# Kernel optimization log

Hardware: AMD Instinct MI355X
Metric: run time of the kernel (lower is better)

The kernel has to match this reference:

```python
import jax, jax.numpy as jnp
import numpy as np


def setup_inputs() -> dict:
    key = jax.random.key(0)
    ks = jax.random.split(key, 7)
    B, S, H, T = 128, 512, 768, 3
    return {
        "inputs": jax.random.normal(ks[0], (B, S, H), dtype=jnp.float32),
        "y": jax.random.randint(ks[1], (B, S), 0, T, dtype=jnp.int64),
        "W": jax.random.normal(ks[2], (T, H), dtype=jnp.float32) * 0.02,
        "b": jax.random.normal(ks[3], (T,), dtype=jnp.float32) * 0.02,
        "transitions": jax.random.normal(ks[4], (T, T), dtype=jnp.float32),
        "start_transitions": jax.random.normal(ks[5], (T,), dtype=jnp.float32),
        "stop_transitions": jax.random.normal(ks[6], (T,), dtype=jnp.float32),
    }


def _crf_loss(feats, tags, transitions, start_transitions, stop_transitions):
    # feats: (B, S, T) emissions; tags: (B, S) int labels
    B, S, T = feats.shape
    # ---- gold sequence score ----
    emit = jnp.take_along_axis(feats, tags[:, :, None], axis=2)[..., 0]  # (B, S)
    trans = transitions[tags[:, :-1], tags[:, 1:]]                        # (B, S-1)
    seq_score = (emit.sum(-1) + trans.sum(-1)
                 + start_transitions[tags[:, 0]]
                 + stop_transitions[tags[:, -1]])                          # (B,)
    # ---- log partition via forward algorithm (scan over time) ----
    a0 = feats[:, 0] + start_transitions[None, :]  # (B, T)

    def step(a, feat_t):
        # a: (B, T) alpha at t-1; feat_t: (B, T) emissions at t
        # scores[b, i, j] = a[b, i] + transitions[i, j] + feat_t[b, j]
        a_new = jax.nn.logsumexp(a[:, :, None] + transitions[None, :, :]
                                 + feat_t[:, None, :], axis=1)
        return a_new, None

    aT, _ = jax.lax.scan(step, a0, jnp.swapaxes(feats[:, 1:], 0, 1))
    log_z = jax.nn.logsumexp(aT + stop_transitions[None, :], axis=1)  # (B,)
    return -(seq_score - log_z).mean()


def reference(inputs, y, W, b, transitions, start_transitions, stop_transitions):
    # Linear projection: (B, S, H) @ (H, T) + (T,)
    prediction = jnp.einsum("bsh,th->bst", inputs, W) + b
    crf_loss = _crf_loss(prediction, y, transitions, start_transitions,
                         stop_transitions)
    return (prediction, crf_loss)
```

## Files before the change

kernel.cpp:

```cpp
#include <hip/hip_runtime.h>

constexpr int NB = 128;
constexpr int NS = 512;
constexpr int NH = 768;
constexpr int NT = 3;
constexpr int ROWS = NB * NS;
constexpr int NCH = 64;
constexpr int CHL = 8;
constexpr float NEG = -1e30f;

__device__ __forceinline__ float lse3(float x0, float x1, float x2) {
    float m = fmaxf(x0, fmaxf(x1, x2));
    return m + __logf(__expf(x0 - m) + __expf(x1 - m) + __expf(x2 - m));
}

__device__ __forceinline__ float dot4(float4 a, float4 b) {
    return a.x * b.x + a.y * b.y + a.z * b.z + a.w * b.w;
}

__device__ __forceinline__ float sel3(int t, float a, float b, float c) {
    return (t == 0) ? a : ((t == 1) ? b : c);
}

__global__ __launch_bounds__(256) void pred_kernel(
    const float* __restrict__ x, const float* __restrict__ W,
    const float* __restrict__ bias, float* __restrict__ out)
{
    const int lane = threadIdx.x & 63;
    const int gw   = blockIdx.x * 4 + (threadIdx.x >> 6);
    const int nw   = gridDim.x * 4;
    const int stride = nw * 2;

    const float4* W4 = (const float4*)W;
    float4 w[3][3];
#pragma unroll
    for (int t = 0; t < 3; ++t)
#pragma unroll
        for (int c = 0; c < 3; ++c)
            w[t][c] = W4[t * 192 + c * 64 + lane];
    const float b0 = bias[0], b1 = bias[1], b2 = bias[2];

    const float4* X4 = (const float4*)x;
    int row = gw * 2;
    if (row >= ROWS) return;

    float4 vA[3], vB[3];
    {
        const int ba = row * 192 + lane;
#pragma unroll
        for (int c = 0; c < 3; ++c) { vA[c] = X4[ba + c * 64]; vB[c] = X4[ba + 192 + c * 64]; }
    }

    while (true) {
        const int nrow = row + stride;
        const bool more = nrow < ROWS;
        float4 tA[3], tB[3];
        if (more) {
            const int nb = nrow * 192 + lane;
#pragma unroll
            for (int c = 0; c < 3; ++c) { tA[c] = X4[nb + c * 64]; tB[c] = X4[nb + 192 + c * 64]; }
        }
        float a0 = dot4(vA[0], w[0][0]) + dot4(vA[1], w[0][1]) + dot4(vA[2], w[0][2]);
        float a1 = dot4(vA[0], w[1][0]) + dot4(vA[1], w[1][1]) + dot4(vA[2], w[1][2]);
        float a2 = dot4(vA[0], w[2][0]) + dot4(vA[1], w[2][1]) + dot4(vA[2], w[2][2]);
        float c0 = dot4(vB[0], w[0][0]) + dot4(vB[1], w[0][1]) + dot4(vB[2], w[0][2]);
        float c1 = dot4(vB[0], w[1][0]) + dot4(vB[1], w[1][1]) + dot4(vB[2], w[1][2]);
        float c2 = dot4(vB[0], w[2][0]) + dot4(vB[1], w[2][1]) + dot4(vB[2], w[2][2]);

        float r0 = a0 + __shfl_xor(a0, 32, 64);
        float s0 = c0 + __shfl_xor(c0, 32, 64);
        float w0 = (lane & 32) ? s0 : r0;
        float r1 = a1 + __shfl_xor(a1, 32, 64);
        float s1 = c1 + __shfl_xor(c1, 32, 64);
        float w1 = (lane & 32) ? s1 : r1;
        float r2 = a2 + __shfl_xor(a2, 32, 64);
        float s2 = c2 + __shfl_xor(c2, 32, 64);
        float w2 = (lane & 32) ? s2 : r2;
        float p0 = w0 + __shfl_xor(w0, 16, 64);
        float p1 = w1 + __shfl_xor(w1, 16, 64);
        float z  = (lane & 16) ? p1 : p0;
#pragma unroll
        for (int off = 8; off >= 1; off >>= 1)
            z += __shfl_xor(z, off, 64);
#pragma unroll
        for (int off = 16; off >= 1; off >>= 1)
            w2 += __shfl_xor(w2, off, 64);

        if ((lane & 15) == 0) {
            const int t = (lane >> 4) & 1;
            const int r = lane >> 5;
            out[(size_t)row * 3 + r * 3 + t] = z + ((t == 0) ? b0 : b1);
        }
        if ((lane & 31) == 0) {
            const int r = lane >> 5;
            out[(size_t)row * 3 + r * 3 + 2] = w2 + b2;
        }
        if (!more) break;
#pragma unroll
        for (int c = 0; c < 3; ++c) { vA[c] = tA[c]; vB[c] = tB[c]; }
        row = nrow;
    }
}

__global__ __launch_bounds__(256) void crf_scan_kernel(
    const float* __restrict__ feats, const int* __restrict__ y,
    const float* __restrict__ trans, float* __restrict__ ws_m,
    float* __restrict__ ws_p)
{
    __shared__ float sTr[9];
    if (threadIdx.x < 9) sTr[threadIdx.x] = trans[threadIdx.x];
    __syncthreads();

    const int gtid = blockIdx.x * 256 + threadIdx.x;
    const int e  = gtid % 3;
    const int bc = gtid / 3;
    const int b  = bc >> 6;
    const int c  = bc & 63;

    const float T00 = sTr[0], T01 = sTr[1], T02 = sTr[2];
    const float T10 = sTr[3], T11 = sTr[4], T12 = sTr[5];
    const float T20 = sTr[6], T21 = sTr[7], T22 = sTr[8];

    const float* fb = feats + (size_t)b * NS * NT;
    const int*   yb = y + b * NS;

    float ff[24];
    {
        float4* fv = (float4*)ff;
        const float4* src = (const float4*)(fb + c * CHL * NT);
#pragma unroll
        for (int i = 0; i < 6; ++i) fv[i] = src[i];
    }
    int yy[8];
    {
        int4* yv = (int4*)yy;
        const int4* ys = (const int4*)(yb + c * CHL);
        yv[0] = ys[0]; yv[1] = ys[1];
    }

    float a0 = (e == 0) ? 0.f : NEG;
    float a1 = (e == 1) ? 0.f : NEG;
    float a2 = (e == 2) ? 0.f : NEG;

    float sc = 0.f;
    int prev;
    if (c == 0) {
        prev = yy[0];
        sc = sel3(prev, ff[0], ff[1], ff[2]);
    } else {
        prev = yb[c * CHL - 1];
    }
    const int sl0 = (c == 0) ? 1 : 0;

#pragma unroll
    for (int sl = 0; sl < CHL; ++sl) {
        if (sl < sl0) continue;
        const float f0 = ff[sl * 3], f1 = ff[sl * 3 + 1], f2 = ff[sl * 3 + 2];
        const int tg = yy[sl];
        sc += sel3(tg, f0, f1, f2) + sTr[prev * 3 + tg];
        prev = tg;
        const float n0 = f0 + lse3(a0 + T00, a1 + T10, a2 + T20);
        const float n1 = f1 + lse3(a0 + T01, a1 + T11, a2 + T21);
        const float n2 = f2 + lse3(a0 + T02, a1 + T12, a2 + T22);
        a0 = n0; a1 = n1; a2 = n2;
    }

    float4* dst = (float4*)(ws_m + (size_t)(b * NCH + c) * 12) + e;
    *dst = make_float4(a0, a1, a2, 0.f);
    if (e == 0) ws_p[b * NCH + c] = sc;
}

__global__ __launch_bounds__(128) void crf_combine_kernel(
    const float* __restrict__ feats, const int* __restrict__ y,
    const float* __restrict__ ws_m, const float* __restrict__ ws_p,
    const float* __restrict__ startt, const float* __restrict__ stopt,
    float* __restrict__ loss_out)
{
    __shared__ float partial[2];
    const int b = threadIdx.x;

    const float st0 = startt[0], st1 = startt[1], st2 = startt[2];
    const float sp0 = stopt[0],  sp1 = stopt[1],  sp2 = stopt[2];

    const float* fb = feats + (size_t)b * NS * NT;
    float a0 = fb[0] + st0, a1 = fb[1] + st1, a2 = fb[2] + st2;

    const float4* M = (const float4*)(ws_m + (size_t)b * NCH * 12);
    const float*  P = ws_p + b * NCH;

    float4 m0 = M[0], m1 = M[1], m2 = M[2];
    float  pp = P[0];
    float  sc = 0.f;

#pragma unroll 4
    for (int c = 0; c < NCH; ++c) {
        float4 u0 = m0, u1 = m1, u2 = m2; float up = pp;
        if (c < NCH - 1) {
            u0 = M[(c + 1) * 3]; u1 = M[(c + 1) * 3 + 1]; u2 = M[(c + 1) * 3 + 2];
            up = P[c + 1];
        }
        sc += pp;
        const float n0 = lse3(a0 + m0.x, a1 + m1.x, a2 + m2.x);
        const float n1 = lse3(a0 + m0.y, a1 + m1.y, a2 + m2.y);
        const float n2 = lse3(a0 + m0.z, a1 + m1.z, a2 + m2.z);
        a0 = n0; a1 = n1; a2 = n2;
        m0 = u0; m1 = u1; m2 = u2; pp = up;
    }

    const float logz = lse3(a0 + sp0, a1 + sp1, a2 + sp2);
    const int y0 = y[b * NS], yl = y[b * NS + NS - 1];
    const float seq = sc + ((y0 == 0) ? st0 : ((y0 == 1) ? st1 : st2))
                         + ((yl == 0) ? sp0 : ((yl == 1) ? sp1 : sp2));
    float val = seq - logz;

#pragma unroll
    for (int off = 32; off >= 1; off >>= 1)
        val += __shfl_xor(val, off, 64);
    if ((threadIdx.x & 63) == 0) partial[threadIdx.x >> 6] = val;
    __syncthreads();
    if (threadIdx.x == 0)
        loss_out[0] = -(partial[0] + partial[1]) / (float)NB;
}

extern "C" void kernel_launch(void* const* d_in, const int* in_sizes, int n_in,
                              void* d_out, int out_size, void* d_ws, size_t ws_size,
                              hipStream_t stream)
{
    const float* x      = (const float*)d_in[0];
    const int*   y      = (const int*)d_in[1];
    const float* W      = (const float*)d_in[2];
    const float* bias   = (const float*)d_in[3];
    const float* trans  = (const float*)d_in[4];
    const float* startt = (const float*)d_in[5];
    const float* stopt  = (const float*)d_in[6];

    float* out      = (float*)d_out;
    float* loss_out = out + (size_t)NB * NS * NT;

    float* ws_m = (float*)d_ws;
    float* ws_p = ws_m + (size_t)NB * NCH * 12;

    pred_kernel<<<1024, 256, 0, stream>>>(x, W, bias, out);
    crf_scan_kernel<<<(NB * NCH * 3) / 256, 256, 0, stream>>>(out, y, trans, ws_m, ws_p);
    crf_combine_kernel<<<1, 128, 0, stream>>>(out, y, ws_m, ws_p, startt, stopt, loss_out);
}
```

Before: 320.9 us.

## Fuse CRF chunk scan and combine into one per-batch kernel with atomic loss

Merges the chunked CRF forward scan and the single-block combine into one kernel with one block per batch row. Chunk transfer matrices now stay in shared memory instead of a global workspace. Each block reduces its row serially and adds its share of the loss with an atomicAdd, and pred_kernel zeroes the loss first. This removes a kernel launch and the workspace round trip, but the loss sum order now varies between runs and each block does a serial 64-step combine on one thread.

After: 306.2 us. 1.05x faster.

```diff
diff --git a/kernel.cpp b/kernel.cpp
--- a/kernel.cpp
+++ b/kernel.cpp
@@ -24,8 +24,11 @@
 
 __global__ __launch_bounds__(256) void pred_kernel(
     const float* __restrict__ x, const float* __restrict__ W,
-    const float* __restrict__ bias, float* __restrict__ out)
+    const float* __restrict__ bias, float* __restrict__ out,
+    float* __restrict__ loss_out)
 {
+    if (blockIdx.x == 0 && threadIdx.x == 0) loss_out[0] = 0.f;
+
     const int lane = threadIdx.x & 63;
     const int gw   = blockIdx.x * 4 + (threadIdx.x >> 6);
     const int nw   = gridDim.x * 4;
@@ -102,20 +105,22 @@
     }
 }
 
-__global__ __launch_bounds__(256) void crf_scan_kernel(
+__global__ __launch_bounds__(192) void crf_kernel(
     const float* __restrict__ feats, const int* __restrict__ y,
-    const float* __restrict__ trans, float* __restrict__ ws_m,
-    float* __restrict__ ws_p)
+    const float* __restrict__ trans, const float* __restrict__ startt,
+    const float* __restrict__ stopt, float* __restrict__ loss_out)
 {
-    __shared__ float sTr[9];
-    if (threadIdx.x < 9) sTr[threadIdx.x] = trans[threadIdx.x];
+    __shared__ float  sTr[9];
+    __shared__ float4 sm[NCH][3];
+    __shared__ float  sp[NCH];
+
+    const int tid = threadIdx.x;
+    if (tid < 9) sTr[tid] = trans[tid];
     __syncthreads();
 
-    const int gtid = blockIdx.x * 256 + threadIdx.x;
-    const int e  = gtid % 3;
-    const int bc = gtid / 3;
-    const int b  = bc >> 6;
-    const int c  = bc & 63;
+    const int b = blockIdx.x;
+    const int e = tid % 3;
+    const int c = tid / 3;
 
     const float T00 = sTr[0], T01 = sTr[1], T02 = sTr[2];
     const float T10 = sTr[3], T11 = sTr[4], T12 = sTr[5];
@@ -165,61 +170,32 @@
         a0 = n0; a1 = n1; a2 = n2;
     }
 
-    float4* dst = (float4*)(ws_m + (size_t)(b * NCH + c) * 12) + e;
-    *dst = make_float4(a0, a1, a2, 0.f);
-    if (e == 0) ws_p[b * NCH + c] = sc;
-}
-
-__global__ __launch_bounds__(128) void crf_combine_kernel(
-    const float* __restrict__ feats, const int* __restrict__ y,
-    const float* __restrict__ ws_m, const float* __restrict__ ws_p,
-    const float* __restrict__ startt, const float* __restrict__ stopt,
-    float* __restrict__ loss_out)
-{
-    __shared__ float partial[2];
-    const int b = threadIdx.x;
-
-    const float st0 = startt[0], st1 = startt[1], st2 = startt[2];
-    const float sp0 = stopt[0],  sp1 = stopt[1],  sp2 = stopt[2];
-
-    const float* fb = feats + (size_t)b * NS * NT;
-    float a0 = fb[0] + st0, a1 = fb[1] + st1, a2 = fb[2] + st2;
-
-    const float4* M = (const float4*)(ws_m + (size_t)b * NCH * 12);
-    const float*  P = ws_p + b * NCH;
-
-    float4 m0 = M[0], m1 = M[1], m2 = M[2];
-    float  pp = P[0];
-    float  sc = 0.f;
-
+    sm[c][e] = make_float4(a0, a1, a2, 0.f);
+    if (e == 0) sp[c] = sc;
+    __syncthreads();
+
+    if (tid == 0) {
+        const float st0 = startt[0], st1 = startt[1], st2 = startt[2];
+        const float sp0 = stopt[0],  sp1 = stopt[1],  sp2 = stopt[2];
+
+        float x0 = fb[0] + st0, x1 = fb[1] + st1, x2 = fb[2] + st2;
+        float sct = 0.f;
 #pragma unroll 4
-    for (int c = 0; c < NCH; ++c) {
-        float4 u0 = m0, u1 = m1, u2 = m2; float up = pp;
-        if (c < NCH - 1) {
-            u0 = M[(c + 1) * 3]; u1 = M[(c + 1) * 3 + 1]; u2 = M[(c + 1) * 3 + 2];
-            up = P[c + 1];
-        }
-        sc += pp;
-        const float n0 = lse3(a0 + m0.x, a1 + m1.x, a2 + m2.x);
-        const float n1 = lse3(a0 + m0.y, a1 + m1.y, a2 + m2.y);
-        const float n2 = lse3(a0 + m0.z, a1 + m1.z, a2 + m2.z);
-        a0 = n0; a1 = n1; a2 = n2;
-        m0 = u0; m1 = u1; m2 = u2; pp = up;
-    }
-
-    const float logz = lse3(a0 + sp0, a1 + sp1, a2 + sp2);
-    const int y0 = y[b * NS], yl = y[b * NS + NS - 1];
-    const float seq = sc + ((y0 == 0) ? st0 : ((y0 == 1) ? st1 : st2))
-                         + ((yl == 0) ? sp0 : ((yl == 1) ? sp1 : sp2));
-    float val = seq - logz;
-
-#pragma unroll
-    for (int off = 32; off >= 1; off >>= 1)
-        val += __shfl_xor(val, off, 64);
-    if ((threadIdx.x & 63) == 0) partial[threadIdx.x >> 6] = val;
-    __syncthreads();
-    if (threadIdx.x == 0)
-        loss_out[0] = -(partial[0] + partial[1]) / (float)NB;
+        for (int cc = 0; cc < NCH; ++cc) {
+            const float4 m0 = sm[cc][0], m1 = sm[cc][1], m2 = sm[cc][2];
+            sct += sp[cc];
+            const float n0 = lse3(x0 + m0.x, x1 + m1.x, x2 + m2.x);
+            const float n1 = lse3(x0 + m0.y, x1 + m1.y, x2 + m2.y);
+            const float n2 = lse3(x0 + m0.z, x1 + m1.z, x2 + m2.z);
+            x0 = n0; x1 = n1; x2 = n2;
+        }
+
+        const float logz = lse3(x0 + sp0, x1 + sp1, x2 + sp2);
+        const int y0 = yb[0], yl = yb[NS - 1];
+        const float seq = sct + ((y0 == 0) ? st0 : ((y0 == 1) ? st1 : st2))
+                              + ((yl == 0) ? sp0 : ((yl == 1) ? sp1 : sp2));
+        atomicAdd(loss_out, -(seq - logz) / (float)NB);
+    }
 }
 
 extern "C" void kernel_launch(void* const* d_in, const int* in_sizes, int n_in,
@@ -237,10 +213,6 @@
     float* out      = (float*)d_out;
     float* loss_out = out + (size_t)NB * NS * NT;
 
-    float* ws_m = (float*)d_ws;
-    float* ws_p = ws_m + (size_t)NB * NCH * 12;
-
-    pred_kernel<<<1024, 256, 0, stream>>>(x, W, bias, out);
-    crf_scan_kernel<<<(NB * NCH * 3) / 256, 256, 0, stream>>>(out, y, trans, ws_m, ws_p);
-    crf_combine_kernel<<<1, 128, 0, stream>>>(out, y, ws_m, ws_p, startt, stopt, loss_out);
-}
+    pred_kernel<<<1024, 256, 0, stream>>>(x, W, bias, out, loss_out);
+    crf_kernel<<<NB, 192, 0, stream>>>(out, y, trans, startt, stopt, loss_out);
+}
```
